# Kernel tuning notes

Hardware: AMD Instinct MI355X
Metric: run time of the kernel (lower is better)

The kernel has to match this reference:

```python
import jax, jax.numpy as jnp
import numpy as np

TEMPERATURE = 0.5
LOSS_WEIGHT = 0.2
EPS = 1e-8


def setup_inputs() -> dict:
    key = jax.random.key(0)
    k1, k2 = jax.random.split(key)
    L, B, H = 4, 256, 65536
    hidden_states = jax.random.normal(k1, (L, B, H), dtype=jnp.float32)
    task_type = jax.random.randint(k2, (B,), 0, 16, dtype=jnp.int64)
    return {"hidden_states": hidden_states, "task_type": task_type}


def reference(hidden_states, task_type):
    # hidden_states: [L, B, H] stacked flattened intermediate activations
    # (world_size == 1, so the gathered global states equal the local states)
    L, B, H = hidden_states.shape
    # F.normalize(p=2, dim=2)
    x = hidden_states / jnp.maximum(
        jnp.linalg.norm(hidden_states, axis=2, keepdims=True), 1e-12)

    # pos_mask from task-type equality, diagonal (self-pairs) zeroed
    pos_mask = (task_type[:, None] == task_type[None, :]).astype(x.dtype)
    pos_mask = pos_mask * (1.0 - jnp.eye(B, dtype=x.dtype))  # [B, B]

    # cdist(..., compute_mode='use_mm_for_euclid_dist') ** 2:
    # ||xi||^2 + ||xj||^2 - 2 xi.xj, clamped at 0
    sq = jnp.sum(x * x, axis=2)                      # [L, B]
    dots = jnp.einsum('lbh,lch->lbc', x, x)          # [L, B, B] -- dominant GEMM
    d2 = jnp.maximum(sq[:, :, None] + sq[:, None, :] - 2.0 * dots, 0.0)

    w = jnp.exp(-(d2 / TEMPERATURE))                 # [L, B, B]
    a = jnp.sum(w * pos_mask[None], axis=2)          # [L, B]
    b = jnp.sum(w, axis=2)                           # [L, B]
    per_layer = -jnp.mean(jnp.log((a + EPS) / (b + EPS)), axis=1)  # [L]
    return jnp.sum(per_layer) / L * LOSS_WEIGHT
```

## Files before the change

### kernel.cpp

```cpp
#include <hip/hip_runtime.h>
#include <hip/hip_bf16.h>

#define L_LAYERS 4
#define B_DIM 256
#define H_DIM 65536
#define KC 1024
#define BK 32
#define NKZ (H_DIM / KC)
#define NSLICE (L_LAYERS * NKZ)
#define LDSTR 40

using bf16x8_t = __attribute__((ext_vector_type(8))) short;
using shortx8  = __attribute__((ext_vector_type(8))) short;
using floatx4  = __attribute__((ext_vector_type(4))) float;

__device__ __forceinline__ unsigned short f2bf(float f) {
    unsigned u = __float_as_uint(f);
    return (unsigned short)((u + 0x7fffu + ((u >> 16) & 1u)) >> 16);
}

__global__ __launch_bounds__(512, 2) void gram_kernel(const float* __restrict__ hs,
                                                      float* __restrict__ S) {
    __shared__ short lds[B_DIM * LDSTR];

    const int tid = threadIdx.x;
    const int bx  = blockIdx.x;
    const int l   = bx >> 6;
    const int kz  = bx & (NKZ - 1);

    const int wave = tid >> 6, lane = tid & 63;
    const int wm = wave >> 1;
    const int wn = wave & 1;
    const int mrow = lane & 15, quad = lane >> 4;

    const int r = tid >> 1;
    const int h = tid & 1;
    const float* gp = hs + ((size_t)l * B_DIM + r) * H_DIM + (size_t)kz * KC + h * 16;
    const int ldsw = r * LDSTR + h * 16;

    floatx4 acc[4][8];
#pragma unroll
    for (int i = 0; i < 4; ++i)
#pragma unroll
        for (int j = 0; j < 8; ++j) acc[i][j] = (floatx4)0.0f;

    float4 pv0 = *(const float4*)(gp + 0);
    float4 pv1 = *(const float4*)(gp + 4);
    float4 pv2 = *(const float4*)(gp + 8);
    float4 pv3 = *(const float4*)(gp + 12);

    for (int kt = 0; kt < KC / BK; ++kt) {
        shortx8 w0, w1;
        w0[0] = (short)f2bf(pv0.x); w0[1] = (short)f2bf(pv0.y);
        w0[2] = (short)f2bf(pv0.z); w0[3] = (short)f2bf(pv0.w);
        w0[4] = (short)f2bf(pv1.x); w0[5] = (short)f2bf(pv1.y);
        w0[6] = (short)f2bf(pv1.z); w0[7] = (short)f2bf(pv1.w);
        w1[0] = (short)f2bf(pv2.x); w1[1] = (short)f2bf(pv2.y);
        w1[2] = (short)f2bf(pv2.z); w1[3] = (short)f2bf(pv2.w);
        w1[4] = (short)f2bf(pv3.x); w1[5] = (short)f2bf(pv3.y);
        w1[6] = (short)f2bf(pv3.z); w1[7] = (short)f2bf(pv3.w);
        *(shortx8*)&lds[ldsw]     = w0;
        *(shortx8*)&lds[ldsw + 8] = w1;

        if (kt < KC / BK - 1) {
            const float* gn = gp + (kt + 1) * BK;
            pv0 = *(const float4*)(gn + 0);
            pv1 = *(const float4*)(gn + 4);
            pv2 = *(const float4*)(gn + 8);
            pv3 = *(const float4*)(gn + 12);
        }
        __syncthreads();

        bf16x8_t af[4], bfv[8];
#pragma unroll
        for (int i = 0; i < 4; ++i)
            af[i] = *(const bf16x8_t*)&lds[(wm * 64 + i * 16 + mrow) * LDSTR + quad * 8];
#pragma unroll
        for (int j = 0; j < 8; ++j)
            bfv[j] = *(const bf16x8_t*)&lds[(wn * 128 + j * 16 + mrow) * LDSTR + quad * 8];
#pragma unroll
        for (int i = 0; i < 4; ++i)
#pragma unroll
            for (int j = 0; j < 8; ++j)
                acc[i][j] = __builtin_amdgcn_mfma_f32_16x16x32_bf16(af[i], bfv[j], acc[i][j], 0, 0, 0);
        __syncthreads();
    }

    float* Ssl = S + (size_t)bx * (B_DIM * B_DIM);
#pragma unroll
    for (int i = 0; i < 4; ++i)
#pragma unroll
        for (int j = 0; j < 8; ++j)
#pragma unroll
            for (int rr = 0; rr < 4; ++rr) {
                const int row = wm * 64 + i * 16 + quad * 4 + rr;
                const int col = wn * 128 + j * 16 + mrow;
                Ssl[row * B_DIM + col] = acc[i][j][rr];
            }
}

__global__ __launch_bounds__(256) void reduce_kernel(const float* __restrict__ S,
                                                     float* __restrict__ G) {
    const int li = blockIdx.x;
    const int j  = threadIdx.x;
    const int l  = li >> 8;
    const int i  = li & 255;
    const float* base = S + ((size_t)l * NKZ) * (B_DIM * B_DIM) + i * B_DIM + j;
    float s = 0.0f;
#pragma unroll
    for (int kz = 0; kz < NKZ; ++kz)
        s += base[(size_t)kz * (B_DIM * B_DIM)];
    G[(size_t)li * B_DIM + j] = s;
}

__global__ __launch_bounds__(256) void loss_kernel(const float* __restrict__ G,
                                                   const int* __restrict__ task,
                                                   float* __restrict__ out) {
    const int i = blockIdx.x, l = blockIdx.y, j = threadIdx.x;

    __shared__ int s_odd_nz;
    if (j == 0) s_odd_nz = 0;
    __syncthreads();
    if (j < 128 && task[2 * j + 1] != 0) s_odd_nz = 1;
    __syncthreads();
    const bool is64 = (s_odd_nz == 0);

    const float* Gl = G + (size_t)l * B_DIM * B_DIM;
    const float gij = Gl[i * B_DIM + j];
    const float gii = Gl[i * B_DIM + i];
    const float gjj = Gl[j * B_DIM + j];
    const float nd  = gij * rsqrtf(gii) * rsqrtf(gjj);
    const float d2  = fmaxf(2.0f - 2.0f * nd, 0.0f);
    const float w   = __expf(-2.0f * d2);

    const int ti = is64 ? task[2 * i] : task[i];
    const int tj = is64 ? task[2 * j] : task[j];
    const float pm = (ti == tj && i != j) ? 1.0f : 0.0f;

    float a = w * pm, b = w;
#pragma unroll
    for (int off = 32; off > 0; off >>= 1) {
        a += __shfl_down(a, off);
        b += __shfl_down(b, off);
    }
    __shared__ float sa[4], sb[4];
    const int wv = j >> 6, ln = j & 63;
    if (ln == 0) { sa[wv] = a; sb[wv] = b; }
    __syncthreads();
    if (j == 0) {
        const float A  = sa[0] + sa[1] + sa[2] + sa[3];
        const float Bb = sb[0] + sb[1] + sb[2] + sb[3];
        const float c  = -logf((A + 1e-8f) / (Bb + 1e-8f)) * (0.2f / 1024.0f);
        atomicAdd(out, c);
    }
}

extern "C" void kernel_launch(void* const* d_in, const int* in_sizes, int n_in,
                              void* d_out, int out_size, void* d_ws, size_t ws_size,
                              hipStream_t stream) {
    const float* hs   = (const float*)d_in[0];
    const int*   task = (const int*)d_in[1];
    float*       out  = (float*)d_out;

    float* S = (float*)d_ws;
    float* G = S + (size_t)NSLICE * (B_DIM * B_DIM);

    hipMemsetAsync(out, 0, sizeof(float), stream);

    gram_kernel<<<dim3(NSLICE), dim3(512), 0, stream>>>(hs, S);
    reduce_kernel<<<dim3(L_LAYERS * B_DIM), dim3(256), 0, stream>>>(S, G);
    loss_kernel<<<dim3(B_DIM, L_LAYERS), dim3(256), 0, stream>>>(G, task, out);
}
```

Measured before the change: 406.9 us.

## Store split-K partial Gram tiles in bf16 and double the K step per LDS stage

Partial Gram slices are now written as bf16, transposed, instead of fp32. This halves the workspace write and reread traffic between the gram and reduce kernels, and the reduce kernel unpacks pairs of bf16 values. The K tile also doubles from 32 to 64, which halves the number of barriers per chunk but holds more prefetch registers and uses more LDS. Rounding the partials to bf16 before the sum adds error that could affect the normalized distances on the diagonal.

```diff
diff --git a/kernel.cpp b/kernel.cpp
--- a/kernel.cpp
+++ b/kernel.cpp
@@ -5,13 +5,15 @@
 #define B_DIM 256
 #define H_DIM 65536
 #define KC 1024
-#define BK 32
+#define BK 64
+#define NKT (KC / BK)
 #define NKZ (H_DIM / KC)
 #define NSLICE (L_LAYERS * NKZ)
-#define LDSTR 40
+#define LDSTR 72
 
 using bf16x8_t = __attribute__((ext_vector_type(8))) short;
 using shortx8  = __attribute__((ext_vector_type(8))) short;
+using shortx4  = __attribute__((ext_vector_type(4))) short;
 using floatx4  = __attribute__((ext_vector_type(4))) float;
 
 __device__ __forceinline__ unsigned short f2bf(float f) {
@@ -20,7 +22,7 @@
 }
 
 __global__ __launch_bounds__(512, 2) void gram_kernel(const float* __restrict__ hs,
-                                                      float* __restrict__ S) {
+                                                      short* __restrict__ S) {
     __shared__ short lds[B_DIM * LDSTR];
 
     const int tid = threadIdx.x;
@@ -35,8 +37,8 @@
 
     const int r = tid >> 1;
     const int h = tid & 1;
-    const float* gp = hs + ((size_t)l * B_DIM + r) * H_DIM + (size_t)kz * KC + h * 16;
-    const int ldsw = r * LDSTR + h * 16;
+    const float* gp = hs + ((size_t)l * B_DIM + r) * H_DIM + (size_t)kz * KC + h * 32;
+    const int ldsw = r * LDSTR + h * 32;
 
     floatx4 acc[4][8];
 #pragma unroll
@@ -44,73 +46,81 @@
 #pragma unroll
         for (int j = 0; j < 8; ++j) acc[i][j] = (floatx4)0.0f;
 
-    float4 pv0 = *(const float4*)(gp + 0);
-    float4 pv1 = *(const float4*)(gp + 4);
-    float4 pv2 = *(const float4*)(gp + 8);
-    float4 pv3 = *(const float4*)(gp + 12);
+    float4 pv[8];
+#pragma unroll
+    for (int q = 0; q < 8; ++q) pv[q] = *(const float4*)(gp + q * 4);
 
-    for (int kt = 0; kt < KC / BK; ++kt) {
-        shortx8 w0, w1;
-        w0[0] = (short)f2bf(pv0.x); w0[1] = (short)f2bf(pv0.y);
-        w0[2] = (short)f2bf(pv0.z); w0[3] = (short)f2bf(pv0.w);
-        w0[4] = (short)f2bf(pv1.x); w0[5] = (short)f2bf(pv1.y);
-        w0[6] = (short)f2bf(pv1.z); w0[7] = (short)f2bf(pv1.w);
-        w1[0] = (short)f2bf(pv2.x); w1[1] = (short)f2bf(pv2.y);
-        w1[2] = (short)f2bf(pv2.z); w1[3] = (short)f2bf(pv2.w);
-        w1[4] = (short)f2bf(pv3.x); w1[5] = (short)f2bf(pv3.y);
-        w1[6] = (short)f2bf(pv3.z); w1[7] = (short)f2bf(pv3.w);
-        *(shortx8*)&lds[ldsw]     = w0;
-        *(shortx8*)&lds[ldsw + 8] = w1;
+    for (int kt = 0; kt < NKT; ++kt) {
+#pragma unroll
+        for (int q = 0; q < 4; ++q) {
+            shortx8 w;
+            w[0] = (short)f2bf(pv[2 * q].x);     w[1] = (short)f2bf(pv[2 * q].y);
+            w[2] = (short)f2bf(pv[2 * q].z);     w[3] = (short)f2bf(pv[2 * q].w);
+            w[4] = (short)f2bf(pv[2 * q + 1].x); w[5] = (short)f2bf(pv[2 * q + 1].y);
+            w[6] = (short)f2bf(pv[2 * q + 1].z); w[7] = (short)f2bf(pv[2 * q + 1].w);
+            *(shortx8*)&lds[ldsw + q * 8] = w;
+        }
 
-        if (kt < KC / BK - 1) {
+        if (kt < NKT - 1) {
             const float* gn = gp + (kt + 1) * BK;
-            pv0 = *(const float4*)(gn + 0);
-            pv1 = *(const float4*)(gn + 4);
-            pv2 = *(const float4*)(gn + 8);
-            pv3 = *(const float4*)(gn + 12);
+#pragma unroll
+            for (int q = 0; q < 8; ++q) pv[q] = *(const float4*)(gn + q * 4);
         }
         __syncthreads();
 
-        bf16x8_t af[4], bfv[8];
 #pragma unroll
-        for (int i = 0; i < 4; ++i)
-            af[i] = *(const bf16x8_t*)&lds[(wm * 64 + i * 16 + mrow) * LDSTR + quad * 8];
+        for (int kk = 0; kk < 2; ++kk) {
+            bf16x8_t af[4], bfv[8];
 #pragma unroll
-        for (int j = 0; j < 8; ++j)
-            bfv[j] = *(const bf16x8_t*)&lds[(wn * 128 + j * 16 + mrow) * LDSTR + quad * 8];
-#pragma unroll
-        for (int i = 0; i < 4; ++i)
+            for (int i = 0; i < 4; ++i)
+                af[i] = *(const bf16x8_t*)&lds[(wm * 64 + i * 16 + mrow) * LDSTR + kk * 32 + quad * 8];
 #pragma unroll
             for (int j = 0; j < 8; ++j)
-                acc[i][j] = __builtin_amdgcn_mfma_f32_16x16x32_bf16(af[i], bfv[j], acc[i][j], 0, 0, 0);
+                bfv[j] = *(const bf16x8_t*)&lds[(wn * 128 + j * 16 + mrow) * LDSTR + kk * 32 + quad * 8];
+#pragma unroll
+            for (int i = 0; i < 4; ++i)
+#pragma unroll
+                for (int j = 0; j < 8; ++j)
+                    acc[i][j] = __builtin_amdgcn_mfma_f32_16x16x32_bf16(af[i], bfv[j], acc[i][j], 0, 0, 0);
+        }
         __syncthreads();
     }
 
-    float* Ssl = S + (size_t)bx * (B_DIM * B_DIM);
+    short* Ssl = S + (size_t)bx * (B_DIM * B_DIM);
 #pragma unroll
-    for (int i = 0; i < 4; ++i)
+    for (int i = 0; i < 4; ++i) {
+        const int row0 = wm * 64 + i * 16 + quad * 4;
 #pragma unroll
-        for (int j = 0; j < 8; ++j)
-#pragma unroll
-            for (int rr = 0; rr < 4; ++rr) {
-                const int row = wm * 64 + i * 16 + quad * 4 + rr;
-                const int col = wn * 128 + j * 16 + mrow;
-                Ssl[row * B_DIM + col] = acc[i][j][rr];
-            }
+        for (int j = 0; j < 8; ++j) {
+            const int col = wn * 128 + j * 16 + mrow;
+            shortx4 v;
+            v[0] = (short)f2bf(acc[i][j][0]);
+            v[1] = (short)f2bf(acc[i][j][1]);
+            v[2] = (short)f2bf(acc[i][j][2]);
+            v[3] = (short)f2bf(acc[i][j][3]);
+            *(shortx4*)&Ssl[(size_t)col * B_DIM + row0] = v;
+        }
+    }
 }
 
-__global__ __launch_bounds__(256) void reduce_kernel(const float* __restrict__ S,
+__global__ __launch_bounds__(128) void reduce_kernel(const short* __restrict__ S,
                                                      float* __restrict__ G) {
     const int li = blockIdx.x;
-    const int j  = threadIdx.x;
+    const int j2 = threadIdx.x;
     const int l  = li >> 8;
     const int i  = li & 255;
-    const float* base = S + ((size_t)l * NKZ) * (B_DIM * B_DIM) + i * B_DIM + j;
-    float s = 0.0f;
+    const unsigned* base = (const unsigned*)(S + ((size_t)l * NKZ) * (B_DIM * B_DIM) + i * B_DIM) + j2;
+    float s0 = 0.0f, s1 = 0.0f;
 #pragma unroll
-    for (int kz = 0; kz < NKZ; ++kz)
-        s += base[(size_t)kz * (B_DIM * B_DIM)];
-    G[(size_t)li * B_DIM + j] = s;
+    for (int kz = 0; kz < NKZ; ++kz) {
+        const unsigned u = base[(size_t)kz * (B_DIM * B_DIM / 2)];
+        s0 += __uint_as_float(u << 16);
+        s1 += __uint_as_float(u & 0xffff0000u);
+    }
+    float2 out;
+    out.x = s0;
+    out.y = s1;
+    *(float2*)(G + (size_t)li * B_DIM + 2 * j2) = out;
 }
 
 __global__ __launch_bounds__(256) void loss_kernel(const float* __restrict__ G,
@@ -162,12 +172,12 @@
     const int*   task = (const int*)d_in[1];
     float*       out  = (float*)d_out;
 
-    float* S = (float*)d_ws;
-    float* G = S + (size_t)NSLICE * (B_DIM * B_DIM);
+    short* S = (short*)d_ws;
+    float* G = (float*)(S + (size_t)NSLICE * (B_DIM * B_DIM));
 
     hipMemsetAsync(out, 0, sizeof(float), stream);
 
     gram_kernel<<<dim3(NSLICE), dim3(512), 0, stream>>>(hs, S);
-    reduce_kernel<<<dim3(L_LAYERS * B_DIM), dim3(256), 0, stream>>>(S, G);
+    reduce_kernel<<<dim3(L_LAYERS * B_DIM), dim3(128), 0, stream>>>(S, G);
     loss_kernel<<<dim3(B_DIM, L_LAYERS), dim3(256), 0, stream>>>(G, task, out);
 }
```

Result: slower. 415.5 us (+2.1%).
